# Kernel tuning notes

Measured on AMD Instinct MI355X. Metric: run time of the kernel, lower is better.

## Reference

```python
import jax, jax.numpy as jnp
import numpy as np

N_ELEC, N_ATOMS, FEAT = 2048, 512, 128
N_UP = 1024  # spins = (1024, 1024)
NUM_RBF = 32
DIM = 256
TANH_GAIN = 5.0 / 3.0  # ActivationWithGain assumed: activation(x) * gain (tanh gain)


def setup_inputs() -> dict:
    key = jax.random.key(0)
    k1, k2, k3 = jax.random.split(key, 3)
    h_one_two = jax.random.normal(k1, (N_ELEC, N_ATOMS, FEAT), dtype=jnp.float32)
    r_im_norm = jax.random.uniform(k2, (N_ELEC, N_ATOMS), dtype=jnp.float32) * 10.0
    # GaussRBF params
    mu = jnp.linspace(0, NUM_RBF - 1, NUM_RBF, dtype=jnp.float32)[None, None, :]  # (1,1,K)
    sigma = jnp.ones((1, 1, NUM_RBF), dtype=jnp.float32) * 10.0
    # Dense(dim) on concat of spin means: in = 2*FEAT
    W = jax.random.normal(k3, (2 * FEAT, DIM), dtype=jnp.float32) / np.sqrt(2 * FEAT)
    b = jnp.zeros((DIM,), dtype=jnp.float32)
    return {"h_one_two": h_one_two, "r_im_norm": r_im_norm, "mu": mu, "sigma": sigma, "W": W, "b": b}


def reference(h_one_two, r_im_norm, mu, sigma, W, b):
    # GaussRBF: (E,A,1) vs (1,1,K) -> (E,A,K), mean over K -> (E,A,1)
    d = r_im_norm[..., None] - mu
    rbf = jnp.exp(-(d * d) / jax.nn.softplus(sigma)).mean(-1, keepdims=True)
    h = h_one_two * rbf  # (E,A,F)
    # spin-split mean pooling over electrons
    up = h[:N_UP].mean(0, keepdims=True)   # (1,A,F)
    dn = h[N_UP:].mean(0, keepdims=True)   # (1,A,F)
    atom_emb = jnp.concatenate([up, dn], axis=-1)  # (1,A,2F)
    atom_emb = jnp.tanh(atom_emb @ W + b) * TANH_GAIN  # (1,A,DIM)
    elec_emb = h.mean(1, keepdims=True)  # (E,1,F)
    return atom_emb, elec_emb
```

## Files before the change

### kernel.cpp

```cpp
#include <hip/hip_runtime.h>
#include <cstdint>
#include <cstddef>

#define E_TOT 2048
#define A_TOT 512
#define FEAT  128
#define N_UP  1024
#define K_RBF 32
#define DIM   256

typedef float vfloat4 __attribute__((ext_vector_type(4)));

template <int EB, int AB>
__global__ __launch_bounds__(256) void main_pass(
    const float* __restrict__ h, const float* __restrict__ r_im,
    const float* __restrict__ mu, const float* __restrict__ sigma,
    float* __restrict__ ws_atom,
    float* __restrict__ ws_elec) {
  constexpr int GA = A_TOT / AB;
  constexpr int WA = AB / 4;
  constexpr int NIA = AB / 8;
  static_assert(EB % 2 == 0, "EB even");
  const int bid = blockIdx.x;
  const int g_a = bid % GA, g_e = bid / GA;
  const int e0 = g_e * EB, a0 = g_a * AB;
  const int t = threadIdx.x;
  const int wave = t >> 6, lane = t & 63;
  const int f4 = lane & 31, r_lo = lane >> 5;

  __shared__ float s_mu[K_RBF], s_inv[K_RBF];
  __shared__ float rbf_lds[EB * AB];
  __shared__ float esum_lds[EB * FEAT];

  if (t < K_RBF) {
    s_mu[t] = mu[t];
    float s = sigma[t];
    float sp = (s > 20.0f) ? s : log1pf(__expf(s));
    s_inv[t] = 1.0f / sp;
  }
  __syncthreads();

  for (int i = t; i < EB * FEAT; i += 256) esum_lds[i] = 0.0f;
  for (int i = t; i < EB * AB; i += 256) {
    int e_l = i / AB, a_l = i % AB;
    float rv = r_im[(size_t)(e0 + e_l) * A_TOT + a0 + a_l];
    float acc = 0.0f;
#pragma unroll
    for (int k = 0; k < K_RBF; ++k) {
      float d = rv - s_mu[k];
      acc += __expf(-d * d * s_inv[k]);
    }
    rbf_lds[i] = acc * (1.0f / K_RBF);
  }
  __syncthreads();

  vfloat4 acc[NIA];
#pragma unroll
  for (int i = 0; i < NIA; ++i) acc[i] = (vfloat4)(0.f);

  const float* hbase = h + ((size_t)e0 * A_TOT + a0) * FEAT;
  const int col = wave * WA + r_lo;

  auto ldrow = [&](vfloat4* buf, int e) {
#pragma unroll
    for (int ia = 0; ia < NIA; ++ia) {
      const float* p = hbase + (size_t)e * (A_TOT * FEAT) +
                       (col + ia * 2) * FEAT + f4 * 4;
      buf[ia] = __builtin_nontemporal_load(reinterpret_cast<const vfloat4*>(p));
    }
  };
  auto process = [&](const vfloat4* buf, int e) {
    vfloat4 esum = (vfloat4)(0.f);
#pragma unroll
    for (int ia = 0; ia < NIA; ++ia) {
      float rb = rbf_lds[e * AB + col + ia * 2];
      vfloat4 v = buf[ia] * rb;
      acc[ia] += v;
      esum += v;
    }
    esum.x += __shfl_down(esum.x, 32, 64);
    esum.y += __shfl_down(esum.y, 32, 64);
    esum.z += __shfl_down(esum.z, 32, 64);
    esum.w += __shfl_down(esum.w, 32, 64);
    if (lane < 32) {
      float* p = &esum_lds[e * FEAT + f4 * 4];
      atomicAdd(p + 0, esum.x);
      atomicAdd(p + 1, esum.y);
      atomicAdd(p + 2, esum.z);
      atomicAdd(p + 3, esum.w);
    }
  };

  vfloat4 b0[NIA], b1[NIA];
  ldrow(b0, 0);
#pragma unroll 4
  for (int e = 0; e < EB; e += 2) {
    ldrow(b1, e + 1);
    process(b0, e);
    if (e + 2 < EB) ldrow(b0, e + 2);
    process(b1, e + 1);
  }

  vfloat4* ws_a4 = reinterpret_cast<vfloat4*>(ws_atom);
#pragma unroll
  for (int ia = 0; ia < NIA; ++ia) {
    const int a_l = col + ia * 2;
    ws_a4[((size_t)g_e * A_TOT + a0 + a_l) * 32 + f4] = acc[ia];
  }

  __syncthreads();
  vfloat4* ws_e4 = reinterpret_cast<vfloat4*>(ws_elec);
  const vfloat4* es4 = reinterpret_cast<const vfloat4*>(esum_lds);
#pragma unroll
  for (int i = t; i < EB * 32; i += 256) {
    const int e_l = i >> 5, ff = i & 31;
    ws_e4[((size_t)g_a * E_TOT + e0 + e_l) * 32 + ff] = es4[e_l * 32 + ff];
  }
}

__global__ __launch_bounds__(256) void finals(
    const float* __restrict__ ws_atom, const float* __restrict__ ws_elec,
    const float* __restrict__ W, const float* __restrict__ bias,
    float* __restrict__ out, int ge_total, int slices) {
  const int t = threadIdx.x;
  if (blockIdx.x < A_TOT) {
    const int a = blockIdx.x;
    __shared__ float s_in[2 * FEAT];
    const int spin = t >> 7;
    const int f = t & 127;
    const int gh = ge_total >> 1;
    const int g0 = spin * gh;
    float acc = 0.0f;
#pragma unroll 4
    for (int g = 0; g < gh; ++g) {
      acc += ws_atom[((size_t)(g0 + g) * A_TOT + a) * FEAT + f];
    }
    s_in[t] = acc * (1.0f / (float)N_UP);
    __syncthreads();
    float o = bias[t];
#pragma unroll 4
    for (int k = 0; k < 2 * FEAT; ++k) {
      o += s_in[k] * W[(size_t)k * DIM + t];
    }
    out[(size_t)a * DIM + t] = tanhf(o) * (5.0f / 3.0f);
  } else {
    const int idx = (int)(blockIdx.x - A_TOT) * 256 + t;
    const int n4 = E_TOT * FEAT / 4;
    const vfloat4* in4 = reinterpret_cast<const vfloat4*>(ws_elec);
    vfloat4 s = (vfloat4)(0.f);
    for (int g = 0; g < slices; ++g) {
      s += in4[(size_t)g * n4 + idx];
    }
    s *= (1.0f / (float)A_TOT);
    reinterpret_cast<vfloat4*>(out + (size_t)A_TOT * DIM)[idx] = s;
  }
}

extern "C" void kernel_launch(void* const* d_in, const int* in_sizes, int n_in,
                              void* d_out, int out_size, void* d_ws, size_t ws_size,
                              hipStream_t stream) {
  const float* h     = (const float*)d_in[0];
  const float* r_im  = (const float*)d_in[1];
  const float* mu    = (const float*)d_in[2];
  const float* sigma = (const float*)d_in[3];
  const float* W     = (const float*)d_in[4];
  const float* b     = (const float*)d_in[5];
  float* out = (float*)d_out;

  float* ws_atom = (float*)d_ws;
  const int finals_grid = A_TOT + (E_TOT * FEAT / 4) / 256;

  const size_t needA = ((size_t)(E_TOT / 32) * A_TOT * FEAT +
                        (size_t)(A_TOT / 32) * E_TOT * FEAT) * 4;
  if (ws_size >= needA) {
    constexpr int GE = E_TOT / 32, GA = A_TOT / 32;
    float* ws_elec = ws_atom + (size_t)GE * A_TOT * FEAT;
    main_pass<32, 32><<<GE * GA, 256, 0, stream>>>(h, r_im, mu, sigma, ws_atom, ws_elec);
    finals<<<finals_grid, 256, 0, stream>>>(ws_atom, ws_elec, W, b, out, GE, GA);
  } else {
    constexpr int GE = E_TOT / 64, GA = A_TOT / 64;
    float* ws_elec = ws_atom + (size_t)GE * A_TOT * FEAT;
    main_pass<64, 64><<<GE * GA, 256, 0, stream>>>(h, r_im, mu, sigma, ws_atom, ws_elec);
    finals<<<finals_grid, 256, 0, stream>>>(ws_atom, ws_elec, W, b, out, GE, GA);
  }
}
```

Measured before the change: 136.5 us.

## Widen atom tile to 128 and pipeline h loads in two chunks per electron

Fixes the atom block at 128 atoms per workgroup, so each thread keeps 16 float4 accumulators, and shrinks the electron block to 16 (or 32 on the fallback path). The h stream is loaded as two 8-load chunks per electron and double-buffered across electrons instead of across pairs of rows. The aim is more independent loads in flight per thread and fewer electron-sum LDS atomics per loaded byte. In exchange it raises register pressure and makes the ws_atom partial-sum buffer larger, which finals then has to read back.

```diff
diff --git a/kernel.cpp b/kernel.cpp
--- a/kernel.cpp
+++ b/kernel.cpp
@@ -11,16 +11,14 @@
 
 typedef float vfloat4 __attribute__((ext_vector_type(4)));
 
-template <int EB, int AB>
+template <int EB>
 __global__ __launch_bounds__(256) void main_pass(
     const float* __restrict__ h, const float* __restrict__ r_im,
     const float* __restrict__ mu, const float* __restrict__ sigma,
     float* __restrict__ ws_atom,
     float* __restrict__ ws_elec) {
+  constexpr int AB = 128;
   constexpr int GA = A_TOT / AB;
-  constexpr int WA = AB / 4;
-  constexpr int NIA = AB / 8;
-  static_assert(EB % 2 == 0, "EB even");
   const int bid = blockIdx.x;
   const int g_a = bid % GA, g_e = bid / GA;
   const int e0 = g_e * EB, a0 = g_a * AB;
@@ -54,30 +52,44 @@
   }
   __syncthreads();
 
-  vfloat4 acc[NIA];
+  vfloat4 acc[16];
 #pragma unroll
-  for (int i = 0; i < NIA; ++i) acc[i] = (vfloat4)(0.f);
+  for (int i = 0; i < 16; ++i) acc[i] = (vfloat4)(0.f);
 
-  const float* hbase = h + ((size_t)e0 * A_TOT + a0) * FEAT;
-  const int col = wave * WA + r_lo;
+  const float* hbase = h + ((size_t)e0 * A_TOT + a0) * FEAT +
+                       (wave * 32 + r_lo) * FEAT + f4 * 4;
+  const int arb = wave * 32 + r_lo;
 
-  auto ldrow = [&](vfloat4* buf, int e) {
+  auto ldchunk = [&](vfloat4* buf, int e, int c) {
 #pragma unroll
-    for (int ia = 0; ia < NIA; ++ia) {
+    for (int i = 0; i < 8; ++i) {
       const float* p = hbase + (size_t)e * (A_TOT * FEAT) +
-                       (col + ia * 2) * FEAT + f4 * 4;
-      buf[ia] = __builtin_nontemporal_load(reinterpret_cast<const vfloat4*>(p));
+                       (c * 8 + i) * (2 * FEAT);
+      buf[i] = __builtin_nontemporal_load(reinterpret_cast<const vfloat4*>(p));
     }
   };
-  auto process = [&](const vfloat4* buf, int e) {
-    vfloat4 esum = (vfloat4)(0.f);
+
+  vfloat4 esum;
+  auto prchunk = [&](vfloat4* buf, int e, int c) {
 #pragma unroll
-    for (int ia = 0; ia < NIA; ++ia) {
-      float rb = rbf_lds[e * AB + col + ia * 2];
-      vfloat4 v = buf[ia] * rb;
-      acc[ia] += v;
+    for (int i = 0; i < 8; ++i) {
+      const int j = c * 8 + i;
+      float rb = rbf_lds[e * AB + arb + j * 2];
+      vfloat4 v = buf[i] * rb;
+      acc[j] += v;
       esum += v;
     }
+  };
+
+  vfloat4 B0[8], B1[8];
+  ldchunk(B0, 0, 0);
+  ldchunk(B1, 0, 1);
+  for (int e = 0; e < EB; ++e) {
+    esum = (vfloat4)(0.f);
+    prchunk(B0, e, 0);
+    if (e + 1 < EB) ldchunk(B0, e + 1, 0);
+    prchunk(B1, e, 1);
+    if (e + 1 < EB) ldchunk(B1, e + 1, 1);
     esum.x += __shfl_down(esum.x, 32, 64);
     esum.y += __shfl_down(esum.y, 32, 64);
     esum.z += __shfl_down(esum.z, 32, 64);
@@ -89,29 +101,18 @@
       atomicAdd(p + 2, esum.z);
       atomicAdd(p + 3, esum.w);
     }
-  };
-
-  vfloat4 b0[NIA], b1[NIA];
-  ldrow(b0, 0);
-#pragma unroll 4
-  for (int e = 0; e < EB; e += 2) {
-    ldrow(b1, e + 1);
-    process(b0, e);
-    if (e + 2 < EB) ldrow(b0, e + 2);
-    process(b1, e + 1);
   }
 
   vfloat4* ws_a4 = reinterpret_cast<vfloat4*>(ws_atom);
 #pragma unroll
-  for (int ia = 0; ia < NIA; ++ia) {
-    const int a_l = col + ia * 2;
-    ws_a4[((size_t)g_e * A_TOT + a0 + a_l) * 32 + f4] = acc[ia];
+  for (int j = 0; j < 16; ++j) {
+    const int a_l = wave * 32 + j * 2 + r_lo;
+    ws_a4[((size_t)g_e * A_TOT + a0 + a_l) * 32 + f4] = acc[j];
   }
 
   __syncthreads();
   vfloat4* ws_e4 = reinterpret_cast<vfloat4*>(ws_elec);
   const vfloat4* es4 = reinterpret_cast<const vfloat4*>(esum_lds);
-#pragma unroll
   for (int i = t; i < EB * 32; i += 256) {
     const int e_l = i >> 5, ff = i & 31;
     ws_e4[((size_t)g_a * E_TOT + e0 + e_l) * 32 + ff] = es4[e_l * 32 + ff];
@@ -169,18 +170,19 @@
 
   float* ws_atom = (float*)d_ws;
   const int finals_grid = A_TOT + (E_TOT * FEAT / 4) / 256;
+  constexpr int GA = 4;
 
-  const size_t needA = ((size_t)(E_TOT / 32) * A_TOT * FEAT +
-                        (size_t)(A_TOT / 32) * E_TOT * FEAT) * 4;
-  if (ws_size >= needA) {
-    constexpr int GE = E_TOT / 32, GA = A_TOT / 32;
+  const size_t need16 = ((size_t)(E_TOT / 16) * A_TOT * FEAT +
+                         (size_t)GA * E_TOT * FEAT) * 4;
+  if (ws_size >= need16) {
+    constexpr int GE = E_TOT / 16;
     float* ws_elec = ws_atom + (size_t)GE * A_TOT * FEAT;
-    main_pass<32, 32><<<GE * GA, 256, 0, stream>>>(h, r_im, mu, sigma, ws_atom, ws_elec);
+    main_pass<16><<<GE * GA, 256, 0, stream>>>(h, r_im, mu, sigma, ws_atom, ws_elec);
     finals<<<finals_grid, 256, 0, stream>>>(ws_atom, ws_elec, W, b, out, GE, GA);
   } else {
-    constexpr int GE = E_TOT / 64, GA = A_TOT / 64;
+    constexpr int GE = E_TOT / 32;
     float* ws_elec = ws_atom + (size_t)GE * A_TOT * FEAT;
-    main_pass<64, 64><<<GE * GA, 256, 0, stream>>>(h, r_im, mu, sigma, ws_atom, ws_elec);
+    main_pass<32><<<GE * GA, 256, 0, stream>>>(h, r_im, mu, sigma, ws_atom, ws_elec);
     finals<<<finals_grid, 256, 0, stream>>>(ws_atom, ws_elec, W, b, out, GE, GA);
   }
 }
```

Result: faster. 129.3 us (-5.3%).
